# Performance work log

Measured on AMD Instinct MI355X. Metric: run time of the kernel, lower is better.

## Reference

```python
import jax, jax.numpy as jnp
import numpy as np

B, N0, FEAT, NHID, GDIM = 32, 2048, 1036, 128, 32
DEG = 16
E = B * N0 * DEG
K1, K2, K3 = 410, 82, 17  # ceil(0.2*{2048,410,82}) per SAGPooling stage


def _segsum(v, idx, n):
    return jax.ops.segment_sum(v, idx, num_segments=n)


def sage_conv(x, src, dst, em, Wl, bl, Wr, n):
    # PyG SAGEConv: lin_l(mean_{j->i} x_j) + lin_r(x_i); lin applied before the
    # (linear) mean -> identical math, messages are NHID-dim not FEAT-dim.
    h = x @ Wl
    s = _segsum(h[src] * em[:, None], dst, n)
    cnt = _segsum(em, dst, n)
    return s / jnp.maximum(cnt, 1.0)[:, None] + bl + x @ Wr


def gcn_score(x, src, dst, em, W, b, n):
    # 1-channel GCNConv with self-loops and symmetric normalization.
    h = x @ W  # [n, 1]
    deg = 1.0 + _segsum(em, dst, n)  # +1 for self loop
    dis = jax.lax.rsqrt(deg)
    norm = dis[src] * dis[dst] * em
    agg = _segsum(h[src] * norm[:, None], dst, n) + h / deg[:, None]
    return (agg + b)[:, 0]


def sag_pool(x, src, dst, em, W, b, n_per, k):
    # Equal-size graphs -> static top-k per graph; dropped edges masked, not removed.
    nb = x.shape[0] // n_per
    score = gcn_score(x, src, dst, em, W, b, x.shape[0])
    _, idx = jax.lax.top_k(score.reshape(nb, n_per), k)
    perm = (idx + (jnp.arange(nb) * n_per)[:, None]).reshape(-1)
    xn = x[perm] * jnp.tanh(score[perm])[:, None]
    inv = jnp.full((x.shape[0],), -1, jnp.int32).at[perm].set(
        jnp.arange(nb * k, dtype=jnp.int32))
    ns, nd = inv[src], inv[dst]
    emn = em * ((ns >= 0) & (nd >= 0)).astype(em.dtype)
    return xn, jnp.maximum(ns, 0), jnp.maximum(nd, 0), emn


def readout(x, k):
    r = x.reshape(B, k, NHID)
    return jnp.concatenate([r.max(axis=1), r.mean(axis=1)], axis=1)  # [B, 2*NHID]


def graphnet(x, src, dst, W1l, b1l, W1r, Wp1, bp1, W2l, b2l, W2r, Wp2, bp2,
             W3l, b3l, W3r, Wp3, bp3, lin1_w, lin1_b, lin2_w, lin2_b, lin3_w, lin3_b):
    # NormalizeFeaturesV2: first 12 cols / column max
    mx = jnp.max(x[:, :12], axis=0)
    x = jnp.concatenate([x[:, :12] / mx, x[:, 12:]], axis=1)
    em = jnp.ones((E,), x.dtype)

    x = jax.nn.relu(sage_conv(x, src, dst, em, W1l, b1l, W1r, B * N0))
    x, s1, d1, e1 = sag_pool(x, src, dst, em, Wp1, bp1, N0, K1)
    x1 = readout(x, K1)

    x = jax.nn.relu(sage_conv(x, s1, d1, e1, W2l, b2l, W2r, B * K1))
    x, s2, d2, e2 = sag_pool(x, s1, d1, e1, Wp2, bp2, K1, K2)
    x2 = readout(x, K2)

    x = jax.nn.relu(sage_conv(x, s2, d2, e2, W3l, b3l, W3r, B * K2))
    x, s3, d3, e3 = sag_pool(x, s2, d2, e2, Wp3, bp3, K2, K3)
    x3 = readout(x, K3)

    h = x1 + x2 + x3
    h = jax.nn.relu(h @ lin1_w + lin1_b)  # dropout is identity at eval
    features = jax.nn.relu(h @ lin2_w + lin2_b)
    out = features @ lin3_w + lin3_b  # act=None
    return features, out


def setup_inputs():
    key = jax.random.key(0)
    ks = jax.random.split(key, 16)
    x = jax.random.normal(ks[0], (B * N0, FEAT), jnp.float32)
    e = jax.random.randint(ks[1], (2, B, N0 * DEG), 0, N0)
    ei = (e + (jnp.arange(B) * N0)[None, :, None]).reshape(2, -1).astype(jnp.int32)

    def lin(k, fi, fo):
        return (jax.random.normal(k, (fi, fo), jnp.float32) / np.sqrt(fi)).astype(jnp.float32)

    z = lambda *s: jnp.zeros(s, jnp.float32)
    return dict(
        x=x, src=ei[0], dst=ei[1],
        W1l=lin(ks[2], FEAT, NHID), b1l=z(NHID), W1r=lin(ks[3], FEAT, NHID),
        Wp1=lin(ks[4], NHID, 1), bp1=z(1),
        W2l=lin(ks[5], NHID, NHID), b2l=z(NHID), W2r=lin(ks[6], NHID, NHID),
        Wp2=lin(ks[7], NHID, 1), bp2=z(1),
        W3l=lin(ks[8], NHID, NHID), b3l=z(NHID), W3r=lin(ks[9], NHID, NHID),
        Wp3=lin(ks[10], NHID, 1), bp3=z(1),
        lin1_w=lin(ks[11], 2 * NHID, NHID), lin1_b=z(NHID),
        lin2_w=lin(ks[12], NHID, GDIM), lin2_b=z(GDIM),
        lin3_w=lin(ks[13], GDIM, 1), lin3_b=z(1),
    )


def reference(x, src, dst, W1l, b1l, W1r, Wp1, bp1, W2l, b2l, W2r, Wp2, bp2,
              W3l, b3l, W3r, Wp3, bp3, lin1_w, lin1_b, lin2_w, lin2_b, lin3_w, lin3_b):
    return graphnet(x, src, dst, W1l, b1l, W1r, Wp1, bp1, W2l, b2l, W2r, Wp2, bp2,
                    W3l, b3l, W3r, Wp3, bp3, lin1_w, lin1_b, lin2_w, lin2_b,
                    lin3_w, lin3_b)
```

## Files before the change

kernel.cpp:

```cpp
#include <hip/hip_runtime.h>

typedef unsigned int u32;
typedef unsigned short u16;

#define NB 32
#define N0V 2048
#define FEATV 1036
#define EDGESV (NB*N0V*16)
#define KK1 410
#define KK2 82
#define KK3 17
#define NN1 (NB*N0V)
#define NN2 (NB*KK1)
#define NN3 (NB*KK2)
#define NN4 (NB*KK3)
#define KSTEP1 33
#define KSTEP2 4
#define ESTR 32768

typedef __bf16 bf16x8 __attribute__((ext_vector_type(8)));
typedef float f32x4 __attribute__((ext_vector_type(4)));

__device__ inline u16 f2bf(float f){
  u32 u = __float_as_uint(f);
  u32 r = (u + 0x7FFFu + ((u >> 16) & 1u)) >> 16;
  return (u16)r;
}
__device__ inline float bf2f(u16 h){ return __uint_as_float(((u32)h) << 16); }
__device__ inline float dec_ord(u32 u){
  u32 bits = (u & 0x80000000u) ? (u ^ 0x80000000u) : ~u;
  return __uint_as_float(bits);
}
__device__ inline u16 bfbits(__bf16 b){ union{__bf16 f; u16 u;} c; c.f=b; return c.u; }
__device__ inline void cvt4c(float4 v, ushort4& h, ushort4& l){
  __bf16 h0=(__bf16)v.x, h1=(__bf16)v.y, h2=(__bf16)v.z, h3=(__bf16)v.w;
  float r0=v.x-(float)h0, r1=v.y-(float)h1, r2=v.z-(float)h2, r3=v.w-(float)h3;
  h.x=bfbits(h0); h.y=bfbits(h1); h.z=bfbits(h2); h.w=bfbits(h3);
  l.x=bfbits((__bf16)r0); l.y=bfbits((__bf16)r1);
  l.z=bfbits((__bf16)r2); l.w=bfbits((__bf16)r3);
}

__global__ void init_kernel(u32* mx){
  if (threadIdx.x < 12) mx[threadIdx.x] = 0;
}

__global__ void colmax_kernel(const float* __restrict__ x, u32* mx){
  __shared__ float sm[256];
  int t = threadIdx.x;
  int r = blockIdx.x*256 + t;
  const float4* p = (const float4*)(x + (size_t)r*FEATV);
  float4 v0 = p[0], v1 = p[1], v2 = p[2];
  float m[12] = {v0.x,v0.y,v0.z,v0.w, v1.x,v1.y,v1.z,v1.w, v2.x,v2.y,v2.z,v2.w};
  for (int j=0;j<12;j++){
    sm[t] = m[j]; __syncthreads();
    for (int off=128; off>0; off>>=1){ if (t<off) sm[t]=fmaxf(sm[t],sm[t+off]); __syncthreads(); }
    if (t==0){
      u32 b = __float_as_uint(sm[0]);
      u32 u = (b & 0x80000000u) ? ~b : (b | 0x80000000u);
      atomicMax(&mx[j], u);
    }
    __syncthreads();
  }
}

__global__ void wprep_all(const float* __restrict__ W1l, const float* __restrict__ W1r,
                          const float* __restrict__ W2l, const float* __restrict__ W2r,
                          const float* __restrict__ W3l, const float* __restrict__ W3r,
                          const u32* __restrict__ mxo,
                          u16* __restrict__ B1h, u16* __restrict__ B1l,
                          u16* __restrict__ B2h, u16* __restrict__ B2l,
                          u16* __restrict__ B3h, u16* __restrict__ B3l){
  int idx = blockIdx.x*256 + threadIdx.x;
  const float *Wl, *Wr; u16 *oh, *ol; int K, o, scale12;
  if (idx < KSTEP1*8192){ Wl=W1l; Wr=W1r; oh=B1h; ol=B1l; K=FEATV; o=idx; scale12=1; }
  else if (idx < (KSTEP1+KSTEP2)*8192){ Wl=W2l; Wr=W2r; oh=B2h; ol=B2l; K=128; o=idx-KSTEP1*8192; scale12=0; }
  else if (idx < (KSTEP1+2*KSTEP2)*8192){ Wl=W3l; Wr=W3r; oh=B3h; ol=B3l; K=128; o=idx-(KSTEP1+KSTEP2)*8192; scale12=0; }
  else return;
  int kt = o >> 13, r13 = o & 8191;
  int khg = r13 >> 11, n = (r13 >> 3) & 255, kk8 = r13 & 7;
  int k = (kt << 5) + khg*8 + kk8;
  float v = 0.f;
  if (k < K) v = (n < 128) ? Wl[(size_t)k*128 + n] : Wr[(size_t)k*128 + (n-128)];
  if (scale12 && k < 12) v /= dec_ord(mxo[k]);
  u16 h = f2bf(v);
  oh[o] = h;
  ol[o] = f2bf(v - bf2f(h));
}

__launch_bounds__(256, 3)
__global__ void gemm_csr_kernel(const float* __restrict__ A, int lda, int M,
                                int Kvalid, int Ksteps,
                                const u16* __restrict__ Bth, const u16* __restrict__ Btl,
                                float* __restrict__ C,
                                const int* __restrict__ srcE, const int* __restrict__ dstE,
                                const int* ecnt_in, int globalIds, int nperCsr,
                                int* __restrict__ rps, int* __restrict__ rpd,
                                int* __restrict__ adjW){
  __shared__ __align__(16) u16 Ah[2][2048];
  __shared__ __align__(16) u16 Al[2][2048];
  int tid = threadIdx.x;

  if ((int)blockIdx.x < NB){
    int g = blockIdx.x;
    int* cnt  = (int*)&Ah[0][0];
    int* part = (int*)&Al[0][0];
    int ne = ecnt_in ? ecnt_in[g] : ESTR;
    size_t eb = (size_t)g*ESTR;
    for (int i = tid; i < nperCsr; i += 256) cnt[i] = 0;
    __syncthreads();
    int goff = globalIds ? g*nperCsr : 0;
    int addB = globalIds ? 0 : g*nperCsr;
    for (int e = tid; e < ne; e += 256) atomicAdd(&cnt[dstE[eb+e] - goff], 1);
    __syncthreads();
    int chunk = (nperCsr + 255) >> 8;
    int c0 = tid*chunk, ssum = 0;
    for (int u = 0; u < chunk; ++u){ int i = c0+u; if (i < nperCsr) ssum += cnt[i]; }
    part[tid] = ssum;
    __syncthreads();
    for (int off = 1; off < 256; off <<= 1){
      int v = (tid >= off) ? part[tid-off] : 0;
      __syncthreads();
      part[tid] += v;
      __syncthreads();
    }
    int run = part[tid] - ssum;
    for (int u = 0; u < chunk; ++u){
      int i = c0+u;
      if (i < nperCsr){
        int c = cnt[i];
        rps[g*nperCsr + i] = (int)(g*ESTR + run);
        rpd[g*nperCsr + i] = c;
        cnt[i] = run;
        run += c;
      }
    }
    __syncthreads();
    for (int e = tid; e < ne; e += 256){
      int d = dstE[eb+e], s = srcE[eb+e];
      int p = atomicAdd(&cnt[d - goff], 1);
      adjW[eb + p] = s + addB;
    }
    return;
  }

  int row0 = ((int)blockIdx.x - NB) * 64;
  int w = tid >> 6, lane = tid & 63;
  int lr = lane & 15, kh = lane >> 4;

  int p0i = tid, p1i = tid + 256;
  int kg0 = p0i >> 7, rw0 = (p0i & 127) >> 1, hf0 = p0i & 1;
  int kg1 = p1i >> 7, rw1 = (p1i & 127) >> 1, hf1 = p1i & 1;
  int coff0 = kg0*8 + hf0*4, coff1 = kg1*8 + hf1*4;
  const float* pA0 = A + (size_t)(row0 + rw0)*lda + coff0;
  const float* pA1 = A + (size_t)(row0 + rw1)*lda + coff1;
  int wi0 = kg0*512 + rw0*8 + hf0*4;
  int wi1 = kg1*512 + rw1*8 + hf1*4;

  const u16* bph = Bth + kh*2048 + (w*64 + lr)*8;
  const u16* bpl = Btl + kh*2048 + (w*64 + lr)*8;

  f32x4 acc[4][4];
  #pragma unroll
  for (int i=0;i<4;i++)
    #pragma unroll
    for (int j=0;j<4;j++) acc[i][j] = (f32x4){0.f,0.f,0.f,0.f};

  float4 z4 = make_float4(0.f,0.f,0.f,0.f);

#define LOADA(KT, V0, V1) { int k0_ = (KT)<<5; \
    V0 = (k0_ + coff0 < Kvalid) ? *(const float4*)(pA0 + k0_) : z4; \
    V1 = (k0_ + coff1 < Kvalid) ? *(const float4*)(pA1 + k0_) : z4; }

#define CVTWRITE(V0, V1, BUF) { ushort4 h_, l_; \
    cvt4c(V0, h_, l_); *(ushort4*)&Ah[BUF][wi0] = h_; *(ushort4*)&Al[BUF][wi0] = l_; \
    cvt4c(V1, h_, l_); *(ushort4*)&Ah[BUF][wi1] = h_; *(ushort4*)&Al[BUF][wi1] = l_; }

  float4 a0, a1, pp0, pp1;
  LOADA(0, a0, a1);
  LOADA(1, pp0, pp1);
  CVTWRITE(a0, a1, 0);
  asm volatile("s_waitcnt lgkmcnt(0)" ::: "memory");
  __builtin_amdgcn_s_barrier();

  for (int kt = 0; kt < Ksteps; ++kt){
    int cur = kt & 1, nxt = cur ^ 1;
    const u16* bh_p = bph + (size_t)kt*8192;
    const u16* bl_p = bpl + (size_t)kt*8192;
    bf16x8 fbh[4], fbl[4];
    #pragma unroll
    for (int ni=0;ni<4;ni++){
      fbh[ni] = *(const bf16x8*)(bh_p + ni*128);
      fbl[ni] = *(const bf16x8*)(bl_p + ni*128);
    }
    float4 n0 = z4, n1 = z4;
    if (kt+2 < Ksteps) LOADA(kt+2, n0, n1);
    bf16x8 fah[4], fal[4];
    #pragma unroll
    for (int mi=0;mi<4;mi++){
      int idx = kh*512 + (mi*16 + lr)*8;
      fah[mi] = *(const bf16x8*)&Ah[cur][idx];
      fal[mi] = *(const bf16x8*)&Al[cur][idx];
    }
    if (kt+1 < Ksteps) CVTWRITE(pp0, pp1, nxt);
    asm volatile("s_waitcnt lgkmcnt(0)" ::: "memory");
    __builtin_amdgcn_sched_barrier(0);
    __builtin_amdgcn_s_setprio(1);
    #pragma unroll
    for (int mi=0;mi<4;mi++)
      #pragma unroll
      for (int ni=0;ni<4;ni++){
        acc[mi][ni] = __builtin_amdgcn_mfma_f32_16x16x32_bf16(fah[mi], fbh[ni], acc[mi][ni], 0,0,0);
        acc[mi][ni] = __builtin_amdgcn_mfma_f32_16x16x32_bf16(fah[mi], fbl[ni], acc[mi][ni], 0,0,0);
        acc[mi][ni] = __builtin_amdgcn_mfma_f32_16x16x32_bf16(fal[mi], fbh[ni], acc[mi][ni], 0,0,0);
      }
    __builtin_amdgcn_s_setprio(0);
    pp0 = n0; pp1 = n1;
    __builtin_amdgcn_s_barrier();
  }
#undef LOADA
#undef CVTWRITE
  #pragma unroll
  for (int mi=0;mi<4;mi++)
    #pragma unroll
    for (int j=0;j<4;j++){
      int row = row0 + mi*16 + kh*4 + j;
      #pragma unroll
      for (int ni=0;ni<4;ni++){
        int col = w*64 + ni*16 + lr;
        C[(size_t)row*256 + col] = acc[mi][ni][j];
      }
    }
}

__global__ void convfin_w(const float* __restrict__ hcomb, const int* __restrict__ rps,
                          const int* __restrict__ rpd, const int* __restrict__ adj,
                          const float* __restrict__ bl, const float* __restrict__ Wp,
                          float* __restrict__ xout, float* __restrict__ hsc,
                          int nper, int bpg, int xcdMap){
  int b = blockIdx.x, t = threadIdx.x;
  int g, slot;
  if (xcdMap){ int xcd = b & 7, idx = b >> 3; g = xcd + 8*(idx >> 8); slot = idx & 255; }
  else { g = b / bpg; slot = b - g*bpg; }
  int wv = t >> 6, lane = t & 63;
  int sub = lane >> 5, l32 = lane & 31;
  int i = slot*8 + wv*2 + sub;
  if (i >= nper) return;
  int gi = g*nper + i;
  int s = rps[gi], d = rpd[gi];
  float4 a = make_float4(0.f,0.f,0.f,0.f);
  for (int e = s; e < s+d; ++e){
    float4 hj = *(const float4*)(hcomb + (size_t)adj[e]*256 + l32*4);
    a.x += hj.x; a.y += hj.y; a.z += hj.z; a.w += hj.w;
  }
  float invc = 1.0f / fmaxf((float)d, 1.0f);
  float4 hr = *(const float4*)(hcomb + (size_t)gi*256 + 128 + l32*4);
  float4 bb = *(const float4*)(bl + l32*4);
  float4 o;
  o.x = fmaxf(a.x*invc + bb.x + hr.x, 0.f);
  o.y = fmaxf(a.y*invc + bb.y + hr.y, 0.f);
  o.z = fmaxf(a.z*invc + bb.z + hr.z, 0.f);
  o.w = fmaxf(a.w*invc + bb.w + hr.w, 0.f);
  *(float4*)(xout + (size_t)gi*128 + l32*4) = o;
  float4 wp = *(const float4*)(Wp + l32*4);
  float v = o.x*wp.x + o.y*wp.y + o.z*wp.z + o.w*wp.w;
  #pragma unroll
  for (int m = 16; m > 0; m >>= 1) v += __shfl_xor(v, m);
  if (l32 == 0) hsc[gi] = v;
}

__global__ void scoreagg_w(const float* __restrict__ hsc, const int* __restrict__ rps,
                           const int* __restrict__ rpd, const int* __restrict__ adj,
                           const float* __restrict__ bp, int nper, int ntot,
                           u32* __restrict__ su){
  int gi = blockIdx.x*256 + threadIdx.x;
  if (gi >= ntot) return;
  float di = 1.0f + (float)rpd[gi];
  float a = hsc[gi] / di;
  float rdi = rsqrtf(di);
  int s = rps[gi], d = rpd[gi];
  for (int e = s; e < s+d; ++e){
    int j = adj[e];
    a += hsc[j] * rsqrtf(1.0f + (float)rpd[j]) * rdi;
  }
  float sc = a + bp[0];
  u32 b = __float_as_uint(sc);
  su[gi] = (b & 0x80000000u) ? ~b : (b | 0x80000000u);
}

__launch_bounds__(512)
__global__ void topkpool(const u32* __restrict__ suG, const float* __restrict__ xin,
                         int nper, int k,
                         float* __restrict__ xp, float* __restrict__ r,
                         int* __restrict__ invG, int* __restrict__ ecnt_next){
  __shared__ u32 su[2048];
  __shared__ int bins[256], sfx[256];
  __shared__ int slist[416];
  __shared__ int tlist[64];
  __shared__ float smx[512], ssm[512];
  __shared__ u32 spfx;
  __shared__ int srem, ssel, stie;
  int g = blockIdx.x, t = threadIdx.x;
  int gbase = g*nper;
  for (int i = t; i < nper; i += 512){
    su[i] = suG[gbase + i];
    invG[gbase + i] = -1;
  }
  if (t == 0){ spfx = 0; srem = k; ssel = 0; stie = 0; if (ecnt_next) ecnt_next[g] = 0; }
  __syncthreads();
  for (int pass = 0; pass < 4; ++pass){
    int shift = 24 - 8*pass;
    if (t < 256) bins[t] = 0;
    __syncthreads();
    u32 pfx = spfx; int rem = srem;
    for (int i = t; i < nper; i += 512){
      u32 u = su[i];
      if (pass == 0 || (u >> (shift+8)) == (pfx >> (shift+8)))
        atomicAdd(&bins[(u >> shift) & 255], 1);
    }
    __syncthreads();
    if (t < 256) sfx[t] = bins[t];
    __syncthreads();
    for (int off=1; off<256; off<<=1){
      int v = 0;
      if (t < 256 && t + off < 256) v = sfx[t+off];
      __syncthreads();
      if (t < 256) sfx[t] += v;
      __syncthreads();
    }
    if (t < 256){
      int above = (t == 255) ? 0 : sfx[t+1];
      if (sfx[t] >= rem && above < rem){
        spfx = pfx | ((u32)t << shift);
        srem = rem - above;
      }
    }
    __syncthreads();
  }
  u32 th = spfx;
  for (int i = t; i < nper; i += 512)
    if (su[i] > th){ int p = atomicAdd(&ssel, 1); slist[p] = i; }
  __syncthreads();
  for (int i = t; i < nper; i += 512)
    if (su[i] == th){ int q = atomicAdd(&stie, 1); if (q < 64) tlist[q] = i; }
  __syncthreads();
  if (t == 0){
    int p = ssel, need = k - p;
    if (need > 0){
      if (stie <= 64){
        for (int a = 1; a < stie; ++a){
          int v = tlist[a], b2 = a-1;
          while (b2 >= 0 && tlist[b2] > v){ tlist[b2+1] = tlist[b2]; b2--; }
          tlist[b2+1] = v;
        }
        for (int m = 0; m < need; ++m) slist[p+m] = tlist[m];
      } else {
        for (int i = 0; i < nper && p < k; ++i)
          if (su[i] == th) slist[p++] = i;
      }
    }
  }
  __syncthreads();
  int q = t >> 7, c = t & 127;
  float mxv = -3.4e38f, smv = 0.f;
  for (int j = q; j < k; j += 4){
    int li = slist[j];
    float ts = tanhf(dec_ord(su[li]));
    float vv = xin[((size_t)(gbase + li))*128 + c] * ts;
    xp[((size_t)(g*k + j))*128 + c] = vv;
    mxv = fmaxf(mxv, vv); smv += vv;
  }
  smx[t] = mxv; ssm[t] = smv;
  for (int j = t; j < k; j += 512) invG[gbase + slist[j]] = j;
  __syncthreads();
  if (t < 128){
    r[g*256 + t] = fmaxf(fmaxf(smx[t], smx[t+128]), fmaxf(smx[t+256], smx[t+384]));
    r[g*256 + 128 + t] = (ssm[t]+ssm[t+128]+ssm[t+256]+ssm[t+384]) / (float)k;
  }
}

__global__ void compactw(const int* __restrict__ srcE, const int* __restrict__ dstE,
                         const int* ecnt_in, int inGlobal, int nperIn,
                         const int* __restrict__ invG,
                         int* __restrict__ osrc, int* __restrict__ odst,
                         int* __restrict__ cursor){
  int b = blockIdx.x;
  int g = b >> 4, sl = b & 15;
  int ne = ecnt_in ? ecnt_in[g] : ESTR;
  int e0 = sl*2048;
  if (e0 >= ne) return;
  int e1 = min(e0 + 2048, ne);
  size_t eb = (size_t)g*ESTR;
  int gadd = inGlobal ? 0 : g*nperIn;
  for (int e = e0 + threadIdx.x; e < e1; e += 256){
    int s = srcE[eb+e] + gadd, d = dstE[eb+e] + gadd;
    int ns = invG[s], nd = invG[d];
    if (ns >= 0 && nd >= 0){
      int p = atomicAdd(&cursor[g], 1);
      osrc[eb + p] = ns; odst[eb + p] = nd;
    }
  }
}

__global__ void head_kernel(const float* __restrict__ r1, const float* __restrict__ r2,
                            const float* __restrict__ r3,
                            const float* __restrict__ w1, const float* __restrict__ b1,
                            const float* __restrict__ w2, const float* __restrict__ b2,
                            const float* __restrict__ w3, const float* __restrict__ b3,
                            float* __restrict__ out){
  __shared__ float hs[32][256];
  __shared__ float h1[32][128];
  __shared__ float ft[32][32];
  int t = threadIdx.x;
  for (int o = t; o < 32*256; o += 256) hs[o>>8][o&255] = r1[o]+r2[o]+r3[o];
  __syncthreads();
  for (int o = t; o < 32*128; o += 256){
    int i = o >> 7, j = o & 127;
    float a = b1[j];
    for (int c = 0; c < 256; ++c) a += hs[i][c]*w1[c*128 + j];
    h1[i][j] = fmaxf(a, 0.f);
  }
  __syncthreads();
  for (int o = t; o < 32*32; o += 256){
    int i = o >> 5, j = o & 31;
    float a = b2[j];
    for (int c = 0; c < 128; ++c) a += h1[i][c]*w2[c*32 + j];
    float v = fmaxf(a, 0.f);
    ft[i][j] = v;
    out[o] = v;
  }
  __syncthreads();
  if (t < 32){
    float a = b3[0];
    for (int c = 0; c < 32; ++c) a += ft[t][c]*w3[c];
    out[1024 + t] = a;
  }
}

extern "C" void kernel_launch(void* const* d_in, const int* in_sizes, int n_in,
                              void* d_out, int out_size, void* d_ws, size_t ws_size,
                              hipStream_t stream){
  (void)in_sizes; (void)n_in; (void)out_size; (void)ws_size;
  const float* x   = (const float*)d_in[0];
  const int* esrc  = (const int*)d_in[1];
  const int* edst  = (const int*)d_in[2];
  const float* W1l = (const float*)d_in[3];
  const float* b1l = (const float*)d_in[4];
  const float* W1r = (const float*)d_in[5];
  const float* Wp1 = (const float*)d_in[6];
  const float* bp1 = (const float*)d_in[7];
  const float* W2l = (const float*)d_in[8];
  const float* b2l = (const float*)d_in[9];
  const float* W2r = (const float*)d_in[10];
  const float* Wp2 = (const float*)d_in[11];
  const float* bp2 = (const float*)d_in[12];
  const float* W3l = (const float*)d_in[13];
  const float* b3l = (const float*)d_in[14];
  const float* W3r = (const float*)d_in[15];
  const float* Wp3 = (const float*)d_in[16];
  const float* bp3 = (const float*)d_in[17];
  const float* l1w = (const float*)d_in[18];
  const float* l1b = (const float*)d_in[19];
  const float* l2w = (const float*)d_in[20];
  const float* l2b = (const float*)d_in[21];
  const float* l3w = (const float*)d_in[22];
  const float* l3b = (const float*)d_in[23];
  float* out = (float*)d_out;

  char* ws = (char*)d_ws;
  size_t off = 0;
  auto alloc = [&](size_t bytes)->char*{
    char* p = ws + off; off = (off + bytes + 255) & ~(size_t)255; return p;
  };

  u32* mx     = (u32*)alloc(64);
  int* ecnt1g = (int*)alloc(NB*4);
  int* ecnt2g = (int*)alloc(NB*4);
  int* rps   = (int*)alloc((size_t)NN1*4);
  int* rpd   = (int*)alloc((size_t)NN1*4);
  int* adj   = (int*)alloc((size_t)EDGESV*4);
  int* eAs   = (int*)alloc((size_t)EDGESV*4);
  int* eAd   = (int*)alloc((size_t)EDGESV*4);
  int* eBs   = (int*)alloc((size_t)EDGESV*4);
  int* eBd   = (int*)alloc((size_t)EDGESV*4);
  u16* B1h   = (u16*)alloc((size_t)KSTEP1*8192*2);
  u16* B1l   = (u16*)alloc((size_t)KSTEP1*8192*2);
  u16* B2h   = (u16*)alloc((size_t)KSTEP2*8192*2);
  u16* B2l   = (u16*)alloc((size_t)KSTEP2*8192*2);
  u16* B3h   = (u16*)alloc((size_t)KSTEP2*8192*2);
  u16* B3l   = (u16*)alloc((size_t)KSTEP2*8192*2);
  float* hcomb = (float*)alloc((size_t)NN1*256*4);
  float* x1    = (float*)alloc((size_t)NN1*128*4);
  float* x2    = (float*)alloc((size_t)NN2*128*4);
  float* x3    = (float*)alloc((size_t)NN3*128*4);
  float* xp1   = (float*)alloc((size_t)NN2*128*4);
  float* xp2   = (float*)alloc((size_t)NN3*128*4);
  float* xp3   = (float*)alloc((size_t)NN4*128*4);
  float* hsc   = (float*)alloc((size_t)NN1*4);
  u32* suG     = (u32*)alloc((size_t)NN1*4);
  int* invG    = (int*)alloc((size_t)NN1*4);
  float* r1    = (float*)alloc((size_t)32*256*4);
  float* r2    = (float*)alloc((size_t)32*256*4);
  float* r3    = (float*)alloc((size_t)32*256*4);

  init_kernel<<<1, 64, 0, stream>>>(mx);
  colmax_kernel<<<256, 256, 0, stream>>>(x, mx);
  wprep_all<<<((KSTEP1+2*KSTEP2)*8192+255)/256, 256, 0, stream>>>(
      W1l, W1r, W2l, W2r, W3l, W3r, mx, B1h, B1l, B2h, B2l, B3h, B3l);

  gemm_csr_kernel<<<NB + NN1/64, 256, 0, stream>>>(
      x, FEATV, NN1, FEATV, KSTEP1, B1h, B1l, hcomb,
      esrc, edst, nullptr, 1, N0V, rps, rpd, adj);
  convfin_w<<<NN1/8, 256, 0, stream>>>(hcomb, rps, rpd, adj, b1l, Wp1, x1, hsc, N0V, 256, 1);
  scoreagg_w<<<NN1/256, 256, 0, stream>>>(hsc, rps, rpd, adj, bp1, N0V, NN1, suG);
  topkpool<<<NB, 512, 0, stream>>>(suG, x1, N0V, KK1, xp1, r1, invG, ecnt1g);
  compactw<<<NB*16, 256, 0, stream>>>(esrc, edst, nullptr, 1, N0V, invG, eAs, eAd, ecnt1g);

  gemm_csr_kernel<<<NB + (NN2+63)/64, 256, 0, stream>>>(
      xp1, 128, NN2, 128, KSTEP2, B2h, B2l, hcomb,
      eAs, eAd, ecnt1g, 0, KK1, rps, rpd, adj);
  convfin_w<<<NB*52, 256, 0, stream>>>(hcomb, rps, rpd, adj, b2l, Wp2, x2, hsc, KK1, 52, 0);
  scoreagg_w<<<(NN2+255)/256, 256, 0, stream>>>(hsc, rps, rpd, adj, bp2, KK1, NN2, suG);
  topkpool<<<NB, 512, 0, stream>>>(suG, x2, KK1, KK2, xp2, r2, invG, ecnt2g);
  compactw<<<NB*16, 256, 0, stream>>>(eAs, eAd, ecnt1g, 0, KK1, invG, eBs, eBd, ecnt2g);

  gemm_csr_kernel<<<NB + (NN3+63)/64, 256, 0, stream>>>(
      xp2, 128, NN3, 128, KSTEP2, B3h, B3l, hcomb,
      eBs, eBd, ecnt2g, 0, KK2, rps, rpd, adj);
  convfin_w<<<NB*11, 256, 0, stream>>>(hcomb, rps, rpd, adj, b3l, Wp3, x3, hsc, KK2, 11, 0);
  scoreagg_w<<<(NN3+255)/256, 256, 0, stream>>>(hsc, rps, rpd, adj, bp3, KK2, NN3, suG);
  topkpool<<<NB, 512, 0, stream>>>(suG, x3, KK2, KK3, xp3, r3, invG, nullptr);

  head_kernel<<<1, 256, 0, stream>>>(r1, r2, r3, l1w, l1b, l2w, l2b, l3w, l3b, out);
}
```

Before: 588.2 us.

## Double-buffer GEMM B fragments in registers and relax LDS wait

The GEMM main loop is unrolled by two and the high-part B fragments are prefetched one k-step ahead into alternating register sets. The low-part B loads are issued at the top of each step and consumed by a separate final MFMA pass, so their latency overlaps the first MFMAs. The LDS wait before the MFMAs now lets the trailing LDS writes stay outstanding, and the full wait moves to just before the barrier. It also drops the launch-bounds occupancy hint and adds unroll pragmas to the edge-aggregation loops; the extra registers may reduce occupancy.

```diff
diff --git a/kernel.cpp b/kernel.cpp
--- a/kernel.cpp
+++ b/kernel.cpp
@@ -87,7 +87,6 @@
   ol[o] = f2bf(v - bf2f(h));
 }
 
-__launch_bounds__(256, 3)
 __global__ void gemm_csr_kernel(const float* __restrict__ A, int lda, int M,
                                 int Kvalid, int Ksteps,
                                 const u16* __restrict__ Bth, const u16* __restrict__ Btl,
@@ -166,59 +165,76 @@
     for (int j=0;j<4;j++) acc[i][j] = (f32x4){0.f,0.f,0.f,0.f};
 
   float4 z4 = make_float4(0.f,0.f,0.f,0.f);
+  bf16x8 bhA[4], bhB[4], blv[4];
 
 #define LOADA(KT, V0, V1) { int k0_ = (KT)<<5; \
     V0 = (k0_ + coff0 < Kvalid) ? *(const float4*)(pA0 + k0_) : z4; \
     V1 = (k0_ + coff1 < Kvalid) ? *(const float4*)(pA1 + k0_) : z4; }
 
+#define LOADBH(KT, SET) { const u16* p_ = bph + (size_t)(KT)*8192; \
+    _Pragma("unroll") for (int ni_=0;ni_<4;ni_++) SET[ni_] = *(const bf16x8*)(p_ + ni_*128); }
+
+#define LOADBL(KT) { const u16* p_ = bpl + (size_t)(KT)*8192; \
+    _Pragma("unroll") for (int ni_=0;ni_<4;ni_++) blv[ni_] = *(const bf16x8*)(p_ + ni_*128); }
+
 #define CVTWRITE(V0, V1, BUF) { ushort4 h_, l_; \
     cvt4c(V0, h_, l_); *(ushort4*)&Ah[BUF][wi0] = h_; *(ushort4*)&Al[BUF][wi0] = l_; \
     cvt4c(V1, h_, l_); *(ushort4*)&Ah[BUF][wi1] = h_; *(ushort4*)&Al[BUF][wi1] = l_; }
 
+#define BODY(KT, CURSET, NXTSET) { \
+    LOADBL(KT); \
+    if ((KT)+1 < Ksteps) LOADBH((KT)+1, NXTSET); \
+    float4 n0 = z4, n1 = z4; \
+    if ((KT)+2 < Ksteps) LOADA((KT)+2, n0, n1); \
+    int cur_ = (KT) & 1, nxt_ = cur_ ^ 1; \
+    bf16x8 fah[4], fal[4]; \
+    _Pragma("unroll") \
+    for (int mi_=0;mi_<4;mi_++){ \
+      int idx_ = kh*512 + (mi_*16 + lr)*8; \
+      fah[mi_] = *(const bf16x8*)&Ah[cur_][idx_]; \
+      fal[mi_] = *(const bf16x8*)&Al[cur_][idx_]; \
+    } \
+    if ((KT)+1 < Ksteps) CVTWRITE(pp0, pp1, nxt_); \
+    asm volatile("s_waitcnt lgkmcnt(4)" ::: "memory");    \
+    __builtin_amdgcn_sched_barrier(0); \
+    __builtin_amdgcn_s_setprio(1); \
+    _Pragma("unroll") \
+    for (int mi_=0;mi_<4;mi_++) \
+      _Pragma("unroll") \
+      for (int ni_=0;ni_<4;ni_++){ \
+        acc[mi_][ni_] = __builtin_amdgcn_mfma_f32_16x16x32_bf16(fah[mi_], CURSET[ni_], acc[mi_][ni_], 0,0,0); \
+        acc[mi_][ni_] = __builtin_amdgcn_mfma_f32_16x16x32_bf16(fal[mi_], CURSET[ni_], acc[mi_][ni_], 0,0,0); \
+      } \
+    _Pragma("unroll") \
+    for (int mi_=0;mi_<4;mi_++) \
+      _Pragma("unroll") \
+      for (int ni_=0;ni_<4;ni_++) \
+        acc[mi_][ni_] = __builtin_amdgcn_mfma_f32_16x16x32_bf16(fah[mi_], blv[ni_], acc[mi_][ni_], 0,0,0); \
+    __builtin_amdgcn_s_setprio(0); \
+    pp0 = n0; pp1 = n1; \
+    asm volatile("s_waitcnt lgkmcnt(0)" ::: "memory");    \
+    __builtin_amdgcn_s_barrier(); \
+  }
+
   float4 a0, a1, pp0, pp1;
   LOADA(0, a0, a1);
   LOADA(1, pp0, pp1);
+  LOADBH(0, bhA);
   CVTWRITE(a0, a1, 0);
   asm volatile("s_waitcnt lgkmcnt(0)" ::: "memory");
   __builtin_amdgcn_s_barrier();
 
-  for (int kt = 0; kt < Ksteps; ++kt){
-    int cur = kt & 1, nxt = cur ^ 1;
-    const u16* bh_p = bph + (size_t)kt*8192;
-    const u16* bl_p = bpl + (size_t)kt*8192;
-    bf16x8 fbh[4], fbl[4];
-    #pragma unroll
-    for (int ni=0;ni<4;ni++){
-      fbh[ni] = *(const bf16x8*)(bh_p + ni*128);
-      fbl[ni] = *(const bf16x8*)(bl_p + ni*128);
-    }
-    float4 n0 = z4, n1 = z4;
-    if (kt+2 < Ksteps) LOADA(kt+2, n0, n1);
-    bf16x8 fah[4], fal[4];
-    #pragma unroll
-    for (int mi=0;mi<4;mi++){
-      int idx = kh*512 + (mi*16 + lr)*8;
-      fah[mi] = *(const bf16x8*)&Ah[cur][idx];
-      fal[mi] = *(const bf16x8*)&Al[cur][idx];
-    }
-    if (kt+1 < Ksteps) CVTWRITE(pp0, pp1, nxt);
-    asm volatile("s_waitcnt lgkmcnt(0)" ::: "memory");
-    __builtin_amdgcn_sched_barrier(0);
-    __builtin_amdgcn_s_setprio(1);
-    #pragma unroll
-    for (int mi=0;mi<4;mi++)
-      #pragma unroll
-      for (int ni=0;ni<4;ni++){
-        acc[mi][ni] = __builtin_amdgcn_mfma_f32_16x16x32_bf16(fah[mi], fbh[ni], acc[mi][ni], 0,0,0);
-        acc[mi][ni] = __builtin_amdgcn_mfma_f32_16x16x32_bf16(fah[mi], fbl[ni], acc[mi][ni], 0,0,0);
-        acc[mi][ni] = __builtin_amdgcn_mfma_f32_16x16x32_bf16(fal[mi], fbh[ni], acc[mi][ni], 0,0,0);
-      }
-    __builtin_amdgcn_s_setprio(0);
-    pp0 = n0; pp1 = n1;
-    __builtin_amdgcn_s_barrier();
-  }
+  int kt = 0;
+  for (; kt+1 < Ksteps; kt += 2){
+    BODY(kt,   bhA, bhB);
+    BODY(kt+1, bhB, bhA);
+  }
+  if (kt < Ksteps) BODY(kt, bhA, bhB);
 #undef LOADA
+#undef LOADBH
+#undef LOADBL
 #undef CVTWRITE
+#undef BODY
   #pragma unroll
   for (int mi=0;mi<4;mi++)
     #pragma unroll
@@ -248,6 +264,7 @@
   int gi = g*nper + i;
   int s = rps[gi], d = rpd[gi];
   float4 a = make_float4(0.f,0.f,0.f,0.f);
+  #pragma unroll 4
   for (int e = s; e < s+d; ++e){
     float4 hj = *(const float4*)(hcomb + (size_t)adj[e]*256 + l32*4);
     a.x += hj.x; a.y += hj.y; a.z += hj.z; a.w += hj.w;
@@ -278,6 +295,7 @@
   float a = hsc[gi] / di;
   float rdi = rsqrtf(di);
   int s = rps[gi], d = rpd[gi];
+  #pragma unroll 4
   for (int e = s; e < s+d; ++e){
     int j = adj[e];
     a += hsc[j] * rsqrtf(1.0f + (float)rpd[j]) * rdi;
@@ -515,7 +533,7 @@
   topkpool<<<NB, 512, 0, stream>>>(suG, x1, N0V, KK1, xp1, r1, invG, ecnt1g);
   compactw<<<NB*16, 256, 0, stream>>>(esrc, edst, nullptr, 1, N0V, invG, eAs, eAd, ecnt1g);
 
-  gemm_csr_kernel<<<NB + (NN2+63)/64, 256, 0, stream>>>(
+  gemm_csr_kernel<<<NB + NN2/64, 256, 0, stream>>>(
       xp1, 128, NN2, 128, KSTEP2, B2h, B2l, hcomb,
       eAs, eAd, ecnt1g, 0, KK1, rps, rpd, adj);
   convfin_w<<<NB*52, 256, 0, stream>>>(hcomb, rps, rpd, adj, b2l, Wp2, x2, hsc, KK1, 52, 0);
@@ -523,7 +541,7 @@
   topkpool<<<NB, 512, 0, stream>>>(suG, x2, KK1, KK2, xp2, r2, invG, ecnt2g);
   compactw<<<NB*16, 256, 0, stream>>>(eAs, eAd, ecnt1g, 0, KK1, invG, eBs, eBd, ecnt2g);
 
-  gemm_csr_kernel<<<NB + (NN3+63)/64, 256, 0, stream>>>(
+  gemm_csr_kernel<<<NB + NN3/64, 256, 0, stream>>>(
       xp2, 128, NN3, 128, KSTEP2, B3h, B3l, hcomb,
       eBs, eBd, ecnt2g, 0, KK2, rps, rpd, adj);
   convfin_w<<<NB*11, 256, 0, stream>>>(hcomb, rps, rpd, adj, b3l, Wp3, x3, hsc, KK2, 11, 0);
```

After: 1.280 ms. 2.18x slower.
